# Kernel optimization log

Measured on AMD Instinct MI355X. Metric: run time of the kernel, lower is better.

Reference implementation:

```python
import jax, jax.numpy as jnp
import numpy as np

B = 64          # number of jets
LVLS = 13       # tree levels (complete binary tree, 4096 leaves/jet)
F = 7           # input features
H = 64          # hidden size
SIZES = [B * (2 ** j) for j in range(LVLS)]
OFFS = np.concatenate([[0], np.cumsum(SIZES)])  # level offsets into flat contents


def setup_inputs() -> dict:
    key = jax.random.key(0)
    ks = jax.random.split(key, 9)
    n_total = int(OFFS[-1])  # 524224
    s = lambda k, shp, fan: jax.random.normal(k, shp, jnp.float32) / np.sqrt(fan)
    return {
        "contents": jax.random.normal(ks[0], (n_total, F), jnp.float32),
        "W_u": s(ks[1], (H, F), F),       "b_u": jnp.zeros((H,), jnp.float32),
        "W_r": s(ks[2], (3 * H, 3 * H), 3 * H), "b_r": jnp.zeros((3 * H,), jnp.float32),
        "W_h": s(ks[3], (H, 3 * H), 3 * H),     "b_h": jnp.zeros((H,), jnp.float32),
        "W_z": s(ks[4], (4 * H, 4 * H), 4 * H), "b_z": jnp.zeros((4 * H,), jnp.float32),
    }


def reference(contents, W_u, b_u, W_r, b_r, W_h, b_h, W_z, b_z):
    # Bottom-up recursive gated embedding (n_iters=0 path -> relu activation).
    up = None  # embedding of level j+1
    for j in reversed(range(LVLS)):
        c = contents[int(OFFS[j]):int(OFFS[j + 1])]        # [n_j, F]
        u = jax.nn.relu(c @ W_u.T + b_u)                   # [n_j, H]
        if j == LVLS - 1:
            up = u                                         # leaf level: no inners
            continue
        n = SIZES[j]
        # children of node k are (2k, 2k+1) at level j+1 -> strided gather
        h_L = up[0::2]                                     # [n_j, H]
        h_R = up[1::2]                                     # [n_j, H]
        hhu = jnp.concatenate([h_L, h_R, u], axis=1)       # [n_j, 3H]
        r = jax.nn.sigmoid(hhu @ W_r.T + b_r)              # reset gate
        h_H = jax.nn.relu((r * hhu) @ W_h.T + b_h)         # candidate
        z = jnp.concatenate([h_H, hhu], axis=1) @ W_z.T + b_z  # [n_j, 4H]
        g = jax.nn.softmax(z.reshape(n, 4, H), axis=1)     # softmax over 4 gates
        up = g[:, 0] * h_H + g[:, 1] * h_L + g[:, 2] * h_R + g[:, 3] * u
    return up.reshape(B, -1)                               # [B, H]
```

## Files before the change

### kernel.cpp

```cpp
#include <hip/hip_runtime.h>
#include <hip/hip_bf16.h>


#define LOG2E 1.4426950408889634f
#define OSTR 76

typedef __bf16 bf16x8 __attribute__((ext_vector_type(8)));
typedef float f32x4 __attribute__((ext_vector_type(4)));
typedef unsigned short bfr;

__device__ __forceinline__ float bfr2f(bfr v) { return __uint_as_float(((unsigned)v) << 16); }
__device__ __forceinline__ bfr f2bfr(float f) {
    __hip_bfloat16 h = __float2bfloat16(f);
    return __builtin_bit_cast(bfr, h);
}
__device__ __forceinline__ float fexp2(float x) {
#if __has_builtin(__builtin_amdgcn_exp2f)
    return __builtin_amdgcn_exp2f(x);
#else
    return exp2f(x);
#endif
}
__device__ __forceinline__ float frcp(float x) {
#if __has_builtin(__builtin_amdgcn_rcpf)
    return __builtin_amdgcn_rcpf(x);
#else
    return 1.f / x;
#endif
}

__device__ __forceinline__ int fidx(int Mt, int kt, int q, int ln, int KT) {
    return ((((Mt * KT + kt) * 4 + q) * 16 + ln) * 8);
}

__device__ __host__ __forceinline__ size_t lvloff(int j) {
    return (size_t)((64 << j) - 64) * 64;
}

__device__ __forceinline__ void pack_one(const float* __restrict__ W, bfr* __restrict__ dst,
                                         int d, int K, float scale) {
    int KT = K >> 5;
    int j = d & 7, lnc = (d >> 3) & 15, q = (d >> 7) & 3;
    int t1 = d >> 9;
    int kt = t1 % KT, ntile = t1 / KT;
    int ncol = ntile * 16 + lnc;
    int k = kt * 32 + q * 8 + j;
    dst[d] = f2bfr(W[(size_t)ncol * K + k] * scale);
}

__global__ void convert_weights(const float* __restrict__ Wr, const float* __restrict__ Wh,
                                const float* __restrict__ Wz, const float* __restrict__ Wu,
                                const float* __restrict__ br, const float* __restrict__ bz,
                                bfr* __restrict__ wr, bfr* __restrict__ wh, bfr* __restrict__ wz,
                                bfr* __restrict__ wu,
                                float* __restrict__ brs, float* __restrict__ bzs) {
    int i = blockIdx.x * 256 + threadIdx.x;
    if (i < 36864) pack_one(Wr, wr, i, 192, LOG2E);
    if (i < 12288) pack_one(Wh, wh, i, 192, 1.f);
    if (i < 65536) pack_one(Wz, wz, i, 256, LOG2E);
    if (i < 2048) {
        int j = i & 7, lnc = (i >> 3) & 15, q = (i >> 7) & 3, ntile = i >> 9;
        int k = q * 8 + j, ncol = ntile * 16 + lnc;
        wu[i] = (k < 7) ? f2bfr(Wu[ncol * 7 + k]) : (bfr)0;
    }
    if (i < 192) brs[i] = br[i] * LOG2E;
    if (i < 256) bzs[i] = bz[i] * LOG2E;
}

__device__ __forceinline__ void stage_c(const float* __restrict__ csrc, int rows,
                                        bfr* s_c) {
    const int tid = threadIdx.x;
    for (int t = tid; t < rows * 4; t += 256) {
        int row = t >> 2, qg = t & 3;
        ushort v[8] = {0, 0, 0, 0, 0, 0, 0, 0};
        if (qg == 0) {
            const float* cp = csrc + (size_t)row * 7;
#pragma unroll
            for (int k = 0; k < 7; ++k) v[k] = f2bfr(cp[k]);
        }
        *(uint4*)&s_c[(((row >> 4) * 4 + qg) * 16 + (row & 15)) * 8] = *(const uint4*)v;
    }
}

__device__ __forceinline__ void store_up_coalesced(
    int row0, int rows, bfr* __restrict__ u_io,
    const ushort (&ovv)[4][4], int Mtn, bfr* s_t)
{
    const int tid = threadIdx.x;
    const int lane = tid & 63, w = tid >> 6;
    const int ln = lane & 15, q = lane >> 4;
    const int colbase = w * 16 + q * 4;
    __syncthreads();
#pragma unroll
    for (int Mt = 0; Mt < 4; ++Mt) {
        if (Mt < Mtn) {
            int row = Mt * 16 + ln;
            if (row < rows)
                *(uint2*)&s_t[row * OSTR + colbase] = *(const uint2*)ovv[Mt];
        }
    }
    __syncthreads();
#pragma unroll
    for (int it = 0; it < 2; ++it) {
        int idx = it * 256 + tid;
        int row = idx >> 3, ck = idx & 7;
        if (row < rows)
            *(uint4*)&u_io[(size_t)(row0 + row) * 64 + ck * 8] =
                *(const uint4*)&s_t[row * OSTR + ck * 8];
    }
}

__device__ __forceinline__ void mmu_own(const bfr* s_c, bfr* s_hhu, bf16x8 awu,
                                        f32x4 bu4, int Mtn, int ln, int q,
                                        int colbase) {
#pragma unroll
    for (int Mt = 0; Mt < 4; ++Mt) {
        if (Mt < Mtn) {
            bf16x8 Bc = *(const bf16x8*)&s_c[((Mt * 4 + q) * 16 + ln) * 8];
            f32x4 acc = {0.f, 0.f, 0.f, 0.f};
            acc = __builtin_amdgcn_mfma_f32_16x16x32_bf16(awu, Bc, acc, 0, 0, 0);
            int kk = 128 + colbase;
            int addr = fidx(Mt, kk >> 5, (kk >> 3) & 3, ln, 6) + (kk & 7);
            ushort uv[4];
#pragma unroll
            for (int r = 0; r < 4; ++r) uv[r] = f2bfr(fmaxf(acc[r] + bu4[r], 0.f));
            *(uint2*)&s_hhu[addr] = *(const uint2*)uv;
        }
    }
}

template <bool CHILD_U>
__device__ __forceinline__ void process_level_glob(
    int row0,
    const bfr* __restrict__ ch, const float* __restrict__ c_child,
    const float* __restrict__ c_own, bfr* __restrict__ u_io,
    const bfr* __restrict__ wu, const float* __restrict__ b_u,
    const bfr* __restrict__ wr, const float* __restrict__ brs,
    const bfr* __restrict__ wh, const float* __restrict__ b_h,
    const bfr* __restrict__ wz, const float* __restrict__ bzs,
    bfr* s_hhu, bfr* s_t)
{
    bfr* s_hH = s_t;
    const int tid = threadIdx.x;
    const int lane = tid & 63, w = tid >> 6;
    const int ln = lane & 15, q = lane >> 4;
    const int colbase = w * 16 + q * 4;
    const int rows = 64, Mtn = 4;

    if (!CHILD_U) {
#pragma unroll
        for (int it = 0; it < 4; ++it) {
            int idx = it * 256 + tid;
            int lns = idx & 15, qs = (idx >> 4) & 3, kts = (idx >> 6) & 3, Mts = idx >> 8;
            int row = Mts * 16 + lns;
            int k = kts * 32 + qs * 8;
            const bfr* src = (k < 64)
                ? ch + (size_t)(2 * (row0 + row)) * 64 + k
                : ch + (size_t)(2 * (row0 + row) + 1) * 64 + (k - 64);
            *(uint4*)&s_hhu[fidx(Mts, kts, qs, lns, 6)] = *(const uint4*)src;
        }
    } else {
        stage_c(c_child + (size_t)(2 * row0) * 7, 128, s_t + 2048);
    }
    stage_c(c_own + (size_t)row0 * 7, 64, s_t);
    __syncthreads();

    {
        bf16x8 awu = *(const bf16x8*)&wu[fidx(w, 0, q, ln, 1)];
        f32x4 bu4 = *(const f32x4*)&b_u[colbase];
        if (CHILD_U) {
#pragma unroll
            for (int Mt = 0; Mt < 8; ++Mt) {
                bf16x8 Bc = *(const bf16x8*)&s_t[2048 + (((Mt * 4 + q) * 16 + ln) * 8)];
                f32x4 acc = {0.f, 0.f, 0.f, 0.f};
                acc = __builtin_amdgcn_mfma_f32_16x16x32_bf16(awu, Bc, acc, 0, 0, 0);
                int crow = Mt * 16 + ln;
                int row = crow >> 1;
                int kk = (crow & 1) * 64 + colbase;
                int addr = fidx(row >> 4, kk >> 5, (kk >> 3) & 3, row & 15, 6) + (kk & 7);
                ushort uv[4];
#pragma unroll
                for (int r = 0; r < 4; ++r) uv[r] = f2bfr(fmaxf(acc[r] + bu4[r], 0.f));
                *(uint2*)&s_hhu[addr] = *(const uint2*)uv;
            }
        }
        mmu_own(s_t, s_hhu, awu, bu4, 4, ln, q, colbase);
    }
    __syncthreads();

    {
        bf16x8 Af[3][6];
#pragma unroll
        for (int nt = 0; nt < 3; ++nt)
#pragma unroll
            for (int kt = 0; kt < 6; ++kt)
                Af[nt][kt] = *(const bf16x8*)&wr[fidx(w * 3 + nt, kt, q, ln, 6)];
#pragma unroll
        for (int Mt = 0; Mt < 4; ++Mt) {
            bf16x8 Bf[6];
#pragma unroll
            for (int kt = 0; kt < 6; ++kt)
                Bf[kt] = *(const bf16x8*)&s_hhu[fidx(Mt, kt, q, ln, 6)];
#pragma unroll
            for (int nt = 0; nt < 3; ++nt) {
                int cb1 = (w * 3 + nt) * 16 + q * 4;
                f32x4 acc = {0.f, 0.f, 0.f, 0.f};
#pragma unroll
                for (int kt = 0; kt < 6; ++kt)
                    acc = __builtin_amdgcn_mfma_f32_16x16x32_bf16(Af[nt][kt], Bf[kt], acc, 0, 0, 0);
                f32x4 br4 = *(const f32x4*)&brs[cb1];
                int addr = fidx(Mt, cb1 >> 5, (cb1 >> 3) & 3, ln, 6) + (cb1 & 7);
                ushort hh[4], tt[4];
                *(uint2*)hh = *(const uint2*)&s_hhu[addr];
#pragma unroll
                for (int r = 0; r < 4; ++r) {
                    float e = fexp2(-(acc[r] + br4[r]));
                    tt[r] = f2bfr(frcp(1.f + e) * bfr2f(hh[r]));
                }
                *(uint2*)&s_t[addr] = *(const uint2*)tt;
            }
        }
    }
    __syncthreads();

    f32x4 hacc[4];
    {
        bf16x8 Ah[6];
#pragma unroll
        for (int kt = 0; kt < 6; ++kt)
            Ah[kt] = *(const bf16x8*)&wh[fidx(w, kt, q, ln, 6)];
#pragma unroll
        for (int Mt = 0; Mt < 4; ++Mt) {
            f32x4 acc = {0.f, 0.f, 0.f, 0.f};
#pragma unroll
            for (int kt = 0; kt < 6; ++kt) {
                bf16x8 Bf = *(const bf16x8*)&s_t[fidx(Mt, kt, q, ln, 6)];
                acc = __builtin_amdgcn_mfma_f32_16x16x32_bf16(Ah[kt], Bf, acc, 0, 0, 0);
            }
            hacc[Mt] = acc;
        }
    }
    __syncthreads();
    {
        f32x4 bh4 = *(const f32x4*)&b_h[colbase];
#pragma unroll
        for (int Mt = 0; Mt < 4; ++Mt) {
            int addr = fidx(Mt, colbase >> 5, (colbase >> 3) & 3, ln, 2) + (colbase & 7);
            ushort hv[4];
#pragma unroll
            for (int r = 0; r < 4; ++r) hv[r] = f2bfr(fmaxf(hacc[Mt][r] + bh4[r], 0.f));
            *(uint2*)&s_hH[addr] = *(const uint2*)hv;
        }
    }
    __syncthreads();

    {
        f32x4 az[4][4];
#pragma unroll
        for (int Mt = 0; Mt < 4; ++Mt)
#pragma unroll
            for (int g = 0; g < 4; ++g) az[Mt][g] = (f32x4){0.f, 0.f, 0.f, 0.f};
#pragma unroll
        for (int g = 0; g < 4; ++g) {
            bf16x8 Aw[8];
#pragma unroll
            for (int kt = 0; kt < 8; ++kt)
                Aw[kt] = *(const bf16x8*)&wz[fidx(g * 4 + w, kt, q, ln, 8)];
#pragma unroll
            for (int Mt = 0; Mt < 4; ++Mt) {
                f32x4 acc = az[Mt][g];
                acc = __builtin_amdgcn_mfma_f32_16x16x32_bf16(
                    Aw[0], *(const bf16x8*)&s_hH[fidx(Mt, 0, q, ln, 2)], acc, 0, 0, 0);
                acc = __builtin_amdgcn_mfma_f32_16x16x32_bf16(
                    Aw[1], *(const bf16x8*)&s_hH[fidx(Mt, 1, q, ln, 2)], acc, 0, 0, 0);
#pragma unroll
                for (int kt = 0; kt < 6; ++kt)
                    acc = __builtin_amdgcn_mfma_f32_16x16x32_bf16(
                        Aw[2 + kt], *(const bf16x8*)&s_hhu[fidx(Mt, kt, q, ln, 6)], acc, 0, 0, 0);
                az[Mt][g] = acc;
            }
        }
        f32x4 bz0 = *(const f32x4*)&bzs[colbase];
        f32x4 bz1 = *(const f32x4*)&bzs[64 + colbase];
        f32x4 bz2 = *(const f32x4*)&bzs[128 + colbase];
        f32x4 bz3 = *(const f32x4*)&bzs[192 + colbase];
        ushort ovv[4][4];
#pragma unroll
        for (int Mt = 0; Mt < 4; ++Mt) {
            int aH = fidx(Mt, colbase >> 5, (colbase >> 3) & 3, ln, 2) + (colbase & 7);
            int a0 = fidx(Mt, colbase >> 5, (colbase >> 3) & 3, ln, 6) + (colbase & 7);
            int c1 = 64 + colbase, c2 = 128 + colbase;
            int a1 = fidx(Mt, c1 >> 5, (c1 >> 3) & 3, ln, 6) + (c1 & 7);
            int a2 = fidx(Mt, c2 >> 5, (c2 >> 3) & 3, ln, 6) + (c2 & 7);
            ushort hHv[4], u0[4], u1[4], u2[4];
            *(uint2*)hHv = *(const uint2*)&s_hH[aH];
            *(uint2*)u0 = *(const uint2*)&s_hhu[a0];
            *(uint2*)u1 = *(const uint2*)&s_hhu[a1];
            *(uint2*)u2 = *(const uint2*)&s_hhu[a2];
#pragma unroll
            for (int r = 0; r < 4; ++r) {
                float e0 = fexp2(az[Mt][0][r] + bz0[r]);
                float e1 = fexp2(az[Mt][1][r] + bz1[r]);
                float e2 = fexp2(az[Mt][2][r] + bz2[r]);
                float e3 = fexp2(az[Mt][3][r] + bz3[r]);
                float inv = frcp(e0 + e1 + e2 + e3);
                float v = (e0 * bfr2f(hHv[r]) + e1 * bfr2f(u0[r]) +
                           e2 * bfr2f(u1[r]) + e3 * bfr2f(u2[r])) * inv;
                ovv[Mt][r] = f2bfr(v);
            }
        }
        store_up_coalesced(row0, rows, u_io, ovv, Mtn, s_t);
    }
}

__global__ __launch_bounds__(256, 2) void level11_kernel(
    const float* __restrict__ c12, const float* __restrict__ c11,
    bfr* __restrict__ u_io,
    const bfr* __restrict__ wr, const float* __restrict__ brs,
    const bfr* __restrict__ wh, const float* __restrict__ b_h,
    const bfr* __restrict__ wz, const float* __restrict__ bzs,
    const bfr* __restrict__ wu, const float* __restrict__ b_u)
{
    __shared__ bfr s_hhu[12288];
    __shared__ bfr s_t[12288];
    process_level_glob<true>(blockIdx.x * 64, nullptr, c12, c11, u_io,
                             wu, b_u, wr, brs, wh, b_h, wz, bzs, s_hhu, s_t);
}

__global__ __launch_bounds__(256, 2) void level_kernel(
    const bfr* __restrict__ ch, const float* __restrict__ c_own,
    bfr* __restrict__ u_io,
    const bfr* __restrict__ wr, const float* __restrict__ brs,
    const bfr* __restrict__ wh, const float* __restrict__ b_h,
    const bfr* __restrict__ wz, const float* __restrict__ bzs,
    const bfr* __restrict__ wu, const float* __restrict__ b_u)
{
    __shared__ bfr s_hhu[12288];
    __shared__ bfr s_t[12288];
    process_level_glob<false>(blockIdx.x * 64, ch, nullptr, c_own, u_io,
                              wu, b_u, wr, brs, wh, b_h, wz, bzs, s_hhu, s_t);
}

__device__ __forceinline__ void load_wregs(
    const bfr* __restrict__ wr, const bfr* __restrict__ wh, const bfr* __restrict__ wz,
    const bfr* __restrict__ wu, int w, int q, int ln,
    bf16x8 (&Af)[3][6], bf16x8 (&Ah)[6], bf16x8 (&Aw)[4][8], bf16x8& awu)
{
#pragma unroll
    for (int nt = 0; nt < 3; ++nt)
#pragma unroll
        for (int kt = 0; kt < 6; ++kt)
            Af[nt][kt] = *(const bf16x8*)&wr[fidx(w * 3 + nt, kt, q, ln, 6)];
#pragma unroll
    for (int kt = 0; kt < 6; ++kt)
        Ah[kt] = *(const bf16x8*)&wh[fidx(w, kt, q, ln, 6)];
#pragma unroll
    for (int g = 0; g < 4; ++g)
#pragma unroll
        for (int kt = 0; kt < 8; ++kt)
            Aw[g][kt] = *(const bf16x8*)&wz[fidx(g * 4 + w, kt, q, ln, 8)];
    awu = *(const bf16x8*)&wu[fidx(w, 0, q, ln, 1)];
}

__device__ __forceinline__ void process_level_regs(
    int row0, int rows,
    const bfr* __restrict__ ch, const float* __restrict__ c_own,
    bfr* __restrict__ u_io,
    const bf16x8 awu, const float* __restrict__ b_u,
    const bf16x8 (&Af)[3][6], const bf16x8 (&Ah)[6], const bf16x8 (&Aw)[4][8],
    const float* __restrict__ brs, const float* __restrict__ b_h,
    const float* __restrict__ bzs,
    float* __restrict__ outp, bfr* s_hhu, bfr* s_t)
{
    bfr* s_hH = s_t;
    const int tid = threadIdx.x;
    const int lane = tid & 63, w = tid >> 6;
    const int ln = lane & 15, q = lane >> 4;
    const int Mtn = (rows + 15) >> 4;
    const int colbase = w * 16 + q * 4;

    __syncthreads();

#pragma unroll
    for (int it = 0; it < 4; ++it) {
        int idx = it * 256 + tid;
        int lns = idx & 15, qs = (idx >> 4) & 3, kts = (idx >> 6) & 3, Mts = idx >> 8;
        int row = Mts * 16 + lns;
        if (row < rows) {
            int k = kts * 32 + qs * 8;
            const bfr* src = (k < 64)
                ? ch + (size_t)(2 * (row0 + row)) * 64 + k
                : ch + (size_t)(2 * (row0 + row) + 1) * 64 + (k - 64);
            *(uint4*)&s_hhu[fidx(Mts, kts, qs, lns, 6)] = *(const uint4*)src;
        }
    }
    stage_c(c_own + (size_t)row0 * 7, rows, s_t);
    __syncthreads();

    {
        f32x4 bu4 = *(const f32x4*)&b_u[colbase];
        mmu_own(s_t, s_hhu, awu, bu4, Mtn, ln, q, colbase);
    }
    __syncthreads();

#pragma unroll
    for (int Mt = 0; Mt < 4; ++Mt) {
        if (Mt < Mtn) {
            bf16x8 Bf[6];
#pragma unroll
            for (int kt = 0; kt < 6; ++kt)
                Bf[kt] = *(const bf16x8*)&s_hhu[fidx(Mt, kt, q, ln, 6)];
#pragma unroll
            for (int nt = 0; nt < 3; ++nt) {
                int cb1 = (w * 3 + nt) * 16 + q * 4;
                f32x4 acc = {0.f, 0.f, 0.f, 0.f};
#pragma unroll
                for (int kt = 0; kt < 6; ++kt)
                    acc = __builtin_amdgcn_mfma_f32_16x16x32_bf16(Af[nt][kt], Bf[kt], acc, 0, 0, 0);
                f32x4 br4 = *(const f32x4*)&brs[cb1];
                int addr = fidx(Mt, cb1 >> 5, (cb1 >> 3) & 3, ln, 6) + (cb1 & 7);
                ushort hh[4], tt[4];
                *(uint2*)hh = *(const uint2*)&s_hhu[addr];
#pragma unroll
                for (int r = 0; r < 4; ++r) {
                    float e = fexp2(-(acc[r] + br4[r]));
                    tt[r] = f2bfr(frcp(1.f + e) * bfr2f(hh[r]));
                }
                *(uint2*)&s_t[addr] = *(const uint2*)tt;
            }
        }
    }
    __syncthreads();

    f32x4 hacc[4];
#pragma unroll
    for (int Mt = 0; Mt < 4; ++Mt) {
        if (Mt < Mtn) {
            f32x4 acc = {0.f, 0.f, 0.f, 0.f};
#pragma unroll
            for (int kt = 0; kt < 6; ++kt) {
                bf16x8 Bf = *(const bf16x8*)&s_t[fidx(Mt, kt, q, ln, 6)];
                acc = __builtin_amdgcn_mfma_f32_16x16x32_bf16(Ah[kt], Bf, acc, 0, 0, 0);
            }
            hacc[Mt] = acc;
        }
    }
    __syncthreads();
    {
        f32x4 bh4 = *(const f32x4*)&b_h[colbase];
#pragma unroll
        for (int Mt = 0; Mt < 4; ++Mt) {
            if (Mt < Mtn) {
                int addr = fidx(Mt, colbase >> 5, (colbase >> 3) & 3, ln, 2) + (colbase & 7);
                ushort hv[4];
#pragma unroll
                for (int r = 0; r < 4; ++r) hv[r] = f2bfr(fmaxf(hacc[Mt][r] + bh4[r], 0.f));
                *(uint2*)&s_hH[addr] = *(const uint2*)hv;
            }
        }
    }
    __syncthreads();

    {
        f32x4 bz0 = *(const f32x4*)&bzs[colbase];
        f32x4 bz1 = *(const f32x4*)&bzs[64 + colbase];
        f32x4 bz2 = *(const f32x4*)&bzs[128 + colbase];
        f32x4 bz3 = *(const f32x4*)&bzs[192 + colbase];
        ushort ovv[4][4];
#pragma unroll
        for (int Mt = 0; Mt < 4; ++Mt) {
            if (Mt < Mtn) {
                bf16x8 Az[8];
                Az[0] = *(const bf16x8*)&s_hH[fidx(Mt, 0, q, ln, 2)];
                Az[1] = *(const bf16x8*)&s_hH[fidx(Mt, 1, q, ln, 2)];
#pragma unroll
                for (int kt = 0; kt < 6; ++kt)
                    Az[2 + kt] = *(const bf16x8*)&s_hhu[fidx(Mt, kt, q, ln, 6)];
                f32x4 azg[4];
#pragma unroll
                for (int g = 0; g < 4; ++g) {
                    f32x4 acc = {0.f, 0.f, 0.f, 0.f};
#pragma unroll
                    for (int kt = 0; kt < 8; ++kt)
                        acc = __builtin_amdgcn_mfma_f32_16x16x32_bf16(Aw[g][kt], Az[kt], acc, 0, 0, 0);
                    azg[g] = acc;
                }
                int aH = fidx(Mt, colbase >> 5, (colbase >> 3) & 3, ln, 2) + (colbase & 7);
                int a0 = fidx(Mt, colbase >> 5, (colbase >> 3) & 3, ln, 6) + (colbase & 7);
                int c1 = 64 + colbase, c2 = 128 + colbase;
                int a1 = fidx(Mt, c1 >> 5, (c1 >> 3) & 3, ln, 6) + (c1 & 7);
                int a2 = fidx(Mt, c2 >> 5, (c2 >> 3) & 3, ln, 6) + (c2 & 7);
                int row = Mt * 16 + ln;
                if (row < rows) {
                    ushort hHv[4], u0[4], u1[4], u2[4];
                    *(uint2*)hHv = *(const uint2*)&s_hH[aH];
                    *(uint2*)u0 = *(const uint2*)&s_hhu[a0];
                    *(uint2*)u1 = *(const uint2*)&s_hhu[a1];
                    *(uint2*)u2 = *(const uint2*)&s_hhu[a2];
                    float of[4];
#pragma unroll
                    for (int r = 0; r < 4; ++r) {
                        float e0 = fexp2(azg[0][r] + bz0[r]);
                        float e1 = fexp2(azg[1][r] + bz1[r]);
                        float e2 = fexp2(azg[2][r] + bz2[r]);
                        float e3 = fexp2(azg[3][r] + bz3[r]);
                        float inv = frcp(e0 + e1 + e2 + e3);
                        float v = (e0 * bfr2f(hHv[r]) + e1 * bfr2f(u0[r]) +
                                   e2 * bfr2f(u1[r]) + e3 * bfr2f(u2[r])) * inv;
                        ovv[Mt][r] = f2bfr(v); of[r] = v;
                    }
                    if (outp)
                        *(float4*)&outp[(size_t)(row0 + row) * 64 + colbase] = *(const float4*)of;
                }
            }
        }
        store_up_coalesced(row0, rows, u_io, ovv, Mtn, s_t);
    }
}

__global__ __launch_bounds__(256, 1) void fused_mid_regs(
    const float* __restrict__ contents, bfr* __restrict__ u_all,
    const bfr* __restrict__ wr, const float* __restrict__ brs,
    const bfr* __restrict__ wh, const float* __restrict__ b_h,
    const bfr* __restrict__ wz, const float* __restrict__ bzs,
    const bfr* __restrict__ wu, const float* __restrict__ b_u)
{
    __shared__ bfr s_hhu[12288];
    __shared__ bfr s_t[12288];
    const int tid = threadIdx.x;
    const int lane = tid & 63, w = tid >> 6, ln = lane & 15, q = lane >> 4;
    bf16x8 Af[3][6], Ah[6], Aw[4][8], awu;
    load_wregs(wr, wh, wz, wu, w, q, ln, Af, Ah, Aw, awu);
    for (int j = 8; j >= 2; --j) {
        int rows = 1 << (j - 2);
        const float* c_own = contents + (size_t)((64 << j) - 64) * 7;
        process_level_regs(blockIdx.x * rows, rows,
                           u_all + lvloff(j + 1), c_own, u_all + lvloff(j),
                           awu, b_u, Af, Ah, Aw, brs, b_h, bzs,
                           nullptr, s_hhu, s_t);
    }
}

__global__ __launch_bounds__(256, 1) void fused_tail_regs(
    const float* __restrict__ contents, bfr* __restrict__ u_all,
    const bfr* __restrict__ wr, const float* __restrict__ brs,
    const bfr* __restrict__ wh, const float* __restrict__ b_h,
    const bfr* __restrict__ wz, const float* __restrict__ bzs,
    const bfr* __restrict__ wu, const float* __restrict__ b_u,
    float* __restrict__ outp)
{
    __shared__ bfr s_hhu[12288];
    __shared__ bfr s_t[12288];
    const int tid = threadIdx.x;
    const int lane = tid & 63, w = tid >> 6, ln = lane & 15, q = lane >> 4;
    bf16x8 Af[3][6], Ah[6], Aw[4][8], awu;
    load_wregs(wr, wh, wz, wu, w, q, ln, Af, Ah, Aw, awu);
    for (int j = 1; j >= 0; --j) {
        int rows = 1 << j;
        const float* c_own = contents + (size_t)((64 << j) - 64) * 7;
        process_level_regs(blockIdx.x * rows, rows,
                           u_all + lvloff(j + 1), c_own, u_all + lvloff(j),
                           awu, b_u, Af, Ah, Aw, brs, b_h, bzs,
                           (j == 0) ? outp : nullptr, s_hhu, s_t);
    }
}

extern "C" void kernel_launch(void* const* d_in, const int* in_sizes, int n_in,
                              void* d_out, int out_size, void* d_ws, size_t ws_size,
                              hipStream_t stream) {
    const float* contents = (const float*)d_in[0];
    const float* W_u = (const float*)d_in[1];
    const float* b_u = (const float*)d_in[2];
    const float* W_r = (const float*)d_in[3];
    const float* b_r = (const float*)d_in[4];
    const float* W_h = (const float*)d_in[5];
    const float* b_h = (const float*)d_in[6];
    const float* W_z = (const float*)d_in[7];
    const float* b_z = (const float*)d_in[8];
    float* out = (float*)d_out;

    bfr* u_all = (bfr*)d_ws;
    bfr* wr = u_all + (size_t)524224 * 64;
    bfr* wh = wr + 36864;
    bfr* wz = wh + 12288;
    float* brs = (float*)(wz + 65536);
    float* bzs = brs + 192;
    bfr* wu = (bfr*)(bzs + 256);

    convert_weights<<<256, 256, 0, stream>>>(W_r, W_h, W_z, W_u, b_r, b_z,
                                             wr, wh, wz, wu, brs, bzs);

    const float* c12 = contents + (size_t)((64 << 12) - 64) * 7;
    const float* c11 = contents + (size_t)((64 << 11) - 64) * 7;
    const float* c10 = contents + (size_t)((64 << 10) - 64) * 7;
    const float* c9  = contents + (size_t)((64 << 9) - 64) * 7;

    level11_kernel<<<2048, 256, 0, stream>>>(c12, c11, u_all + lvloff(11),
                                             wr, brs, wh, b_h, wz, bzs, wu, b_u);
    level_kernel<<<1024, 256, 0, stream>>>(u_all + lvloff(11), c10, u_all + lvloff(10),
                                           wr, brs, wh, b_h, wz, bzs, wu, b_u);
    level_kernel<<<512, 256, 0, stream>>>(u_all + lvloff(10), c9, u_all + lvloff(9),
                                          wr, brs, wh, b_h, wz, bzs, wu, b_u);
    fused_mid_regs<<<256, 256, 0, stream>>>(contents, u_all,
                                            wr, brs, wh, b_h, wz, bzs, wu, b_u);
    fused_tail_regs<<<64, 256, 0, stream>>>(contents, u_all,
                                            wr, brs, wh, b_h, wz, bzs, wu, b_u, out);
}
```

Measured before the change: 199.0 us.

## Fuse levels 11, 10 and 9 into one kernel with per-block subtree processing

Merges the three separate level launches into a single kernel. Each block handles 64 rows of level 11, then the 32 parent rows at level 10 and 16 rows at level 9 whose children it produced itself, so no cross-block synchronization is needed. The level routine now takes a row count and skips MFMA tiles beyond it. This removes two launches and their drain gaps and keeps child data hot in cache. In exchange, the later levels run with partially filled tiles, and every block reloads the full weight fragments for each level.

```diff
diff --git a/kernel.cpp b/kernel.cpp
--- a/kernel.cpp
+++ b/kernel.cpp
@@ -131,7 +131,7 @@
 
 template <bool CHILD_U>
 __device__ __forceinline__ void process_level_glob(
-    int row0,
+    int row0, int rows,
     const bfr* __restrict__ ch, const float* __restrict__ c_child,
     const float* __restrict__ c_own, bfr* __restrict__ u_io,
     const bfr* __restrict__ wu, const float* __restrict__ b_u,
@@ -145,7 +145,9 @@
     const int lane = tid & 63, w = tid >> 6;
     const int ln = lane & 15, q = lane >> 4;
     const int colbase = w * 16 + q * 4;
-    const int rows = 64, Mtn = 4;
+    const int Mtn = (rows + 15) >> 4;
+
+    __syncthreads();
 
     if (!CHILD_U) {
 #pragma unroll
@@ -153,16 +155,18 @@
             int idx = it * 256 + tid;
             int lns = idx & 15, qs = (idx >> 4) & 3, kts = (idx >> 6) & 3, Mts = idx >> 8;
             int row = Mts * 16 + lns;
-            int k = kts * 32 + qs * 8;
-            const bfr* src = (k < 64)
-                ? ch + (size_t)(2 * (row0 + row)) * 64 + k
-                : ch + (size_t)(2 * (row0 + row) + 1) * 64 + (k - 64);
-            *(uint4*)&s_hhu[fidx(Mts, kts, qs, lns, 6)] = *(const uint4*)src;
+            if (row < rows) {
+                int k = kts * 32 + qs * 8;
+                const bfr* src = (k < 64)
+                    ? ch + (size_t)(2 * (row0 + row)) * 64 + k
+                    : ch + (size_t)(2 * (row0 + row) + 1) * 64 + (k - 64);
+                *(uint4*)&s_hhu[fidx(Mts, kts, qs, lns, 6)] = *(const uint4*)src;
+            }
         }
     } else {
         stage_c(c_child + (size_t)(2 * row0) * 7, 128, s_t + 2048);
     }
-    stage_c(c_own + (size_t)row0 * 7, 64, s_t);
+    stage_c(c_own + (size_t)row0 * 7, rows, s_t);
     __syncthreads();
 
     {
@@ -184,7 +188,7 @@
                 *(uint2*)&s_hhu[addr] = *(const uint2*)uv;
             }
         }
-        mmu_own(s_t, s_hhu, awu, bu4, 4, ln, q, colbase);
+        mmu_own(s_t, s_hhu, awu, bu4, Mtn, ln, q, colbase);
     }
     __syncthreads();
 
@@ -197,27 +201,29 @@
                 Af[nt][kt] = *(const bf16x8*)&wr[fidx(w * 3 + nt, kt, q, ln, 6)];
 #pragma unroll
         for (int Mt = 0; Mt < 4; ++Mt) {
-            bf16x8 Bf[6];
-#pragma unroll
-            for (int kt = 0; kt < 6; ++kt)
-                Bf[kt] = *(const bf16x8*)&s_hhu[fidx(Mt, kt, q, ln, 6)];
-#pragma unroll
-            for (int nt = 0; nt < 3; ++nt) {
-                int cb1 = (w * 3 + nt) * 16 + q * 4;
-                f32x4 acc = {0.f, 0.f, 0.f, 0.f};
+            if (Mt < Mtn) {
+                bf16x8 Bf[6];
 #pragma unroll
                 for (int kt = 0; kt < 6; ++kt)
-                    acc = __builtin_amdgcn_mfma_f32_16x16x32_bf16(Af[nt][kt], Bf[kt], acc, 0, 0, 0);
-                f32x4 br4 = *(const f32x4*)&brs[cb1];
-                int addr = fidx(Mt, cb1 >> 5, (cb1 >> 3) & 3, ln, 6) + (cb1 & 7);
-                ushort hh[4], tt[4];
-                *(uint2*)hh = *(const uint2*)&s_hhu[addr];
-#pragma unroll
-                for (int r = 0; r < 4; ++r) {
-                    float e = fexp2(-(acc[r] + br4[r]));
-                    tt[r] = f2bfr(frcp(1.f + e) * bfr2f(hh[r]));
+                    Bf[kt] = *(const bf16x8*)&s_hhu[fidx(Mt, kt, q, ln, 6)];
+#pragma unroll
+                for (int nt = 0; nt < 3; ++nt) {
+                    int cb1 = (w * 3 + nt) * 16 + q * 4;
+                    f32x4 acc = {0.f, 0.f, 0.f, 0.f};
+#pragma unroll
+                    for (int kt = 0; kt < 6; ++kt)
+                        acc = __builtin_amdgcn_mfma_f32_16x16x32_bf16(Af[nt][kt], Bf[kt], acc, 0, 0, 0);
+                    f32x4 br4 = *(const f32x4*)&brs[cb1];
+                    int addr = fidx(Mt, cb1 >> 5, (cb1 >> 3) & 3, ln, 6) + (cb1 & 7);
+                    ushort hh[4], tt[4];
+                    *(uint2*)hh = *(const uint2*)&s_hhu[addr];
+#pragma unroll
+                    for (int r = 0; r < 4; ++r) {
+                        float e = fexp2(-(acc[r] + br4[r]));
+                        tt[r] = f2bfr(frcp(1.f + e) * bfr2f(hh[r]));
+                    }
+                    *(uint2*)&s_t[addr] = *(const uint2*)tt;
                 }
-                *(uint2*)&s_t[addr] = *(const uint2*)tt;
             }
         }
     }
@@ -231,13 +237,15 @@
             Ah[kt] = *(const bf16x8*)&wh[fidx(w, kt, q, ln, 6)];
 #pragma unroll
         for (int Mt = 0; Mt < 4; ++Mt) {
-            f32x4 acc = {0.f, 0.f, 0.f, 0.f};
-#pragma unroll
-            for (int kt = 0; kt < 6; ++kt) {
-                bf16x8 Bf = *(const bf16x8*)&s_t[fidx(Mt, kt, q, ln, 6)];
-                acc = __builtin_amdgcn_mfma_f32_16x16x32_bf16(Ah[kt], Bf, acc, 0, 0, 0);
-            }
-            hacc[Mt] = acc;
+            if (Mt < Mtn) {
+                f32x4 acc = {0.f, 0.f, 0.f, 0.f};
+#pragma unroll
+                for (int kt = 0; kt < 6; ++kt) {
+                    bf16x8 Bf = *(const bf16x8*)&s_t[fidx(Mt, kt, q, ln, 6)];
+                    acc = __builtin_amdgcn_mfma_f32_16x16x32_bf16(Ah[kt], Bf, acc, 0, 0, 0);
+                }
+                hacc[Mt] = acc;
+            }
         }
     }
     __syncthreads();
@@ -245,11 +253,13 @@
         f32x4 bh4 = *(const f32x4*)&b_h[colbase];
 #pragma unroll
         for (int Mt = 0; Mt < 4; ++Mt) {
-            int addr = fidx(Mt, colbase >> 5, (colbase >> 3) & 3, ln, 2) + (colbase & 7);
-            ushort hv[4];
-#pragma unroll
-            for (int r = 0; r < 4; ++r) hv[r] = f2bfr(fmaxf(hacc[Mt][r] + bh4[r], 0.f));
-            *(uint2*)&s_hH[addr] = *(const uint2*)hv;
+            if (Mt < Mtn) {
+                int addr = fidx(Mt, colbase >> 5, (colbase >> 3) & 3, ln, 2) + (colbase & 7);
+                ushort hv[4];
+#pragma unroll
+                for (int r = 0; r < 4; ++r) hv[r] = f2bfr(fmaxf(hacc[Mt][r] + bh4[r], 0.f));
+                *(uint2*)&s_hH[addr] = *(const uint2*)hv;
+            }
         }
     }
     __syncthreads();
@@ -268,16 +278,18 @@
                 Aw[kt] = *(const bf16x8*)&wz[fidx(g * 4 + w, kt, q, ln, 8)];
 #pragma unroll
             for (int Mt = 0; Mt < 4; ++Mt) {
-                f32x4 acc = az[Mt][g];
-                acc = __builtin_amdgcn_mfma_f32_16x16x32_bf16(
-                    Aw[0], *(const bf16x8*)&s_hH[fidx(Mt, 0, q, ln, 2)], acc, 0, 0, 0);
-                acc = __builtin_amdgcn_mfma_f32_16x16x32_bf16(
-                    Aw[1], *(const bf16x8*)&s_hH[fidx(Mt, 1, q, ln, 2)], acc, 0, 0, 0);
-#pragma unroll
-                for (int kt = 0; kt < 6; ++kt)
+                if (Mt < Mtn) {
+                    f32x4 acc = az[Mt][g];
                     acc = __builtin_amdgcn_mfma_f32_16x16x32_bf16(
-                        Aw[2 + kt], *(const bf16x8*)&s_hhu[fidx(Mt, kt, q, ln, 6)], acc, 0, 0, 0);
-                az[Mt][g] = acc;
+                        Aw[0], *(const bf16x8*)&s_hH[fidx(Mt, 0, q, ln, 2)], acc, 0, 0, 0);
+                    acc = __builtin_amdgcn_mfma_f32_16x16x32_bf16(
+                        Aw[1], *(const bf16x8*)&s_hH[fidx(Mt, 1, q, ln, 2)], acc, 0, 0, 0);
+#pragma unroll
+                    for (int kt = 0; kt < 6; ++kt)
+                        acc = __builtin_amdgcn_mfma_f32_16x16x32_bf16(
+                            Aw[2 + kt], *(const bf16x8*)&s_hhu[fidx(Mt, kt, q, ln, 6)], acc, 0, 0, 0);
+                    az[Mt][g] = acc;
+                }
             }
         }
         f32x4 bz0 = *(const f32x4*)&bzs[colbase];
@@ -287,35 +299,39 @@
         ushort ovv[4][4];
 #pragma unroll
         for (int Mt = 0; Mt < 4; ++Mt) {
-            int aH = fidx(Mt, colbase >> 5, (colbase >> 3) & 3, ln, 2) + (colbase & 7);
-            int a0 = fidx(Mt, colbase >> 5, (colbase >> 3) & 3, ln, 6) + (colbase & 7);
-            int c1 = 64 + colbase, c2 = 128 + colbase;
-            int a1 = fidx(Mt, c1 >> 5, (c1 >> 3) & 3, ln, 6) + (c1 & 7);
-            int a2 = fidx(Mt, c2 >> 5, (c2 >> 3) & 3, ln, 6) + (c2 & 7);
-            ushort hHv[4], u0[4], u1[4], u2[4];
-            *(uint2*)hHv = *(const uint2*)&s_hH[aH];
-            *(uint2*)u0 = *(const uint2*)&s_hhu[a0];
-            *(uint2*)u1 = *(const uint2*)&s_hhu[a1];
-            *(uint2*)u2 = *(const uint2*)&s_hhu[a2];
-#pragma unroll
-            for (int r = 0; r < 4; ++r) {
-                float e0 = fexp2(az[Mt][0][r] + bz0[r]);
-                float e1 = fexp2(az[Mt][1][r] + bz1[r]);
-                float e2 = fexp2(az[Mt][2][r] + bz2[r]);
-                float e3 = fexp2(az[Mt][3][r] + bz3[r]);
-                float inv = frcp(e0 + e1 + e2 + e3);
-                float v = (e0 * bfr2f(hHv[r]) + e1 * bfr2f(u0[r]) +
-                           e2 * bfr2f(u1[r]) + e3 * bfr2f(u2[r])) * inv;
-                ovv[Mt][r] = f2bfr(v);
+            if (Mt < Mtn) {
+                int aH = fidx(Mt, colbase >> 5, (colbase >> 3) & 3, ln, 2) + (colbase & 7);
+                int a0 = fidx(Mt, colbase >> 5, (colbase >> 3) & 3, ln, 6) + (colbase & 7);
+                int c1 = 64 + colbase, c2 = 128 + colbase;
+                int a1 = fidx(Mt, c1 >> 5, (c1 >> 3) & 3, ln, 6) + (c1 & 7);
+                int a2 = fidx(Mt, c2 >> 5, (c2 >> 3) & 3, ln, 6) + (c2 & 7);
+                int row = Mt * 16 + ln;
+                if (row < rows) {
+                    ushort hHv[4], u0[4], u1[4], u2[4];
+                    *(uint2*)hHv = *(const uint2*)&s_hH[aH];
+                    *(uint2*)u0 = *(const uint2*)&s_hhu[a0];
+                    *(uint2*)u1 = *(const uint2*)&s_hhu[a1];
+                    *(uint2*)u2 = *(const uint2*)&s_hhu[a2];
+#pragma unroll
+                    for (int r = 0; r < 4; ++r) {
+                        float e0 = fexp2(az[Mt][0][r] + bz0[r]);
+                        float e1 = fexp2(az[Mt][1][r] + bz1[r]);
+                        float e2 = fexp2(az[Mt][2][r] + bz2[r]);
+                        float e3 = fexp2(az[Mt][3][r] + bz3[r]);
+                        float inv = frcp(e0 + e1 + e2 + e3);
+                        float v = (e0 * bfr2f(hHv[r]) + e1 * bfr2f(u0[r]) +
+                                   e2 * bfr2f(u1[r]) + e3 * bfr2f(u2[r])) * inv;
+                        ovv[Mt][r] = f2bfr(v);
+                    }
+                }
             }
         }
         store_up_coalesced(row0, rows, u_io, ovv, Mtn, s_t);
     }
 }
 
-__global__ __launch_bounds__(256, 2) void level11_kernel(
-    const float* __restrict__ c12, const float* __restrict__ c11,
-    bfr* __restrict__ u_io,
+__global__ __launch_bounds__(256, 2) void levels_big(
+    const float* __restrict__ contents, bfr* __restrict__ u_all,
     const bfr* __restrict__ wr, const float* __restrict__ brs,
     const bfr* __restrict__ wh, const float* __restrict__ b_h,
     const bfr* __restrict__ wz, const float* __restrict__ bzs,
@@ -323,22 +339,19 @@
 {
     __shared__ bfr s_hhu[12288];
     __shared__ bfr s_t[12288];
-    process_level_glob<true>(blockIdx.x * 64, nullptr, c12, c11, u_io,
-                             wu, b_u, wr, brs, wh, b_h, wz, bzs, s_hhu, s_t);
-}
-
-__global__ __launch_bounds__(256, 2) void level_kernel(
-    const bfr* __restrict__ ch, const float* __restrict__ c_own,
-    bfr* __restrict__ u_io,
-    const bfr* __restrict__ wr, const float* __restrict__ brs,
-    const bfr* __restrict__ wh, const float* __restrict__ b_h,
-    const bfr* __restrict__ wz, const float* __restrict__ bzs,
-    const bfr* __restrict__ wu, const float* __restrict__ b_u)
-{
-    __shared__ bfr s_hhu[12288];
-    __shared__ bfr s_t[12288];
-    process_level_glob<false>(blockIdx.x * 64, ch, nullptr, c_own, u_io,
-                              wu, b_u, wr, brs, wh, b_h, wz, bzs, s_hhu, s_t);
+    const float* c12 = contents + (size_t)((64 << 12) - 64) * 7;
+    const float* c11 = contents + (size_t)((64 << 11) - 64) * 7;
+    const float* c10 = contents + (size_t)((64 << 10) - 64) * 7;
+    const float* c9  = contents + (size_t)((64 << 9) - 64) * 7;
+    process_level_glob<true>((int)blockIdx.x * 64, 64, nullptr, c12, c11,
+                             u_all + lvloff(11), wu, b_u, wr, brs, wh, b_h,
+                             wz, bzs, s_hhu, s_t);
+    process_level_glob<false>((int)blockIdx.x * 32, 32, u_all + lvloff(11),
+                              nullptr, c10, u_all + lvloff(10), wu, b_u,
+                              wr, brs, wh, b_h, wz, bzs, s_hhu, s_t);
+    process_level_glob<false>((int)blockIdx.x * 16, 16, u_all + lvloff(10),
+                              nullptr, c9, u_all + lvloff(9), wu, b_u,
+                              wr, brs, wh, b_h, wz, bzs, s_hhu, s_t);
 }
 
 __device__ __forceinline__ void load_wregs(
@@ -589,18 +602,8 @@
 
     convert_weights<<<256, 256, 0, stream>>>(W_r, W_h, W_z, W_u, b_r, b_z,
                                              wr, wh, wz, wu, brs, bzs);
-
-    const float* c12 = contents + (size_t)((64 << 12) - 64) * 7;
-    const float* c11 = contents + (size_t)((64 << 11) - 64) * 7;
-    const float* c10 = contents + (size_t)((64 << 10) - 64) * 7;
-    const float* c9  = contents + (size_t)((64 << 9) - 64) * 7;
-
-    level11_kernel<<<2048, 256, 0, stream>>>(c12, c11, u_all + lvloff(11),
-                                             wr, brs, wh, b_h, wz, bzs, wu, b_u);
-    level_kernel<<<1024, 256, 0, stream>>>(u_all + lvloff(11), c10, u_all + lvloff(10),
-                                           wr, brs, wh, b_h, wz, bzs, wu, b_u);
-    level_kernel<<<512, 256, 0, stream>>>(u_all + lvloff(10), c9, u_all + lvloff(9),
-                                          wr, brs, wh, b_h, wz, bzs, wu, b_u);
+    levels_big<<<2048, 256, 0, stream>>>(contents, u_all,
+                                         wr, brs, wh, b_h, wz, bzs, wu, b_u);
     fused_mid_regs<<<256, 256, 0, stream>>>(contents, u_all,
                                             wr, brs, wh, b_h, wz, bzs, wu, b_u);
     fused_tail_regs<<<64, 256, 0, stream>>>(contents, u_all,
```

Result: slower. 211.6 us (+6.3%).
